# Kernel tuning notes

Measured on AMD Instinct MI355X. Metric: run time of the kernel, lower is better.

## Reference

```python
import jax, jax.numpy as jnp
import numpy as np

N_NODES = 100000
N_EDGES = 3200000
BATCH = 16
LAYER_NUMBER = 4


def setup_inputs() -> dict:
    key = jax.random.key(0)
    k1, k2, k3, k4 = jax.random.split(key, 4)
    x = jax.random.normal(k1, (N_NODES, BATCH), dtype=jnp.float32)
    # learnable per-edge weights (log1p(counts) at init in the original; the
    # parameter itself is what is learned, so a plain random init is faithful)
    weights = jax.random.normal(k2, (N_EDGES,), dtype=jnp.float32)
    row = jax.random.randint(k3, (N_EDGES,), 0, N_NODES, dtype=jnp.int64)
    col = jax.random.randint(k4, (N_EDGES,), 0, N_NODES, dtype=jnp.int64)
    return {"x": x, "weights": weights, "row": row, "col": col}


def reference(x, weights, row, col):
    # Repeated sparse COO SpMM: y <- A @ y, applied layer_number times,
    # where A[row[e], col[e]] = weights[e].
    def step(y, _):
        msg = weights[:, None] * y[col]                      # [E, B] gather + scale
        y_new = jax.ops.segment_sum(msg, row, num_segments=N_NODES)  # [N, B] scatter-add
        return y_new, None

    y, _ = jax.lax.scan(step, x, None, length=LAYER_NUMBER)
    return y
```

## Files before the change

kernel.cpp:

```cpp
#include <hip/hip_runtime.h>

#define N_NODES 100000
#define N_EDGES 3200000
#define BATCH 16
#define BKT_SHIFT 6
#define BKT_NODES 64
#define K_BUCKETS 1563
#define NB 512
#define SUB (N_EDGES / NB)
#define FT 512
#define SCAN_T 256
#define SCAN_C 7
#define CAP 4096

__global__ void hist_kernel(const int* __restrict__ row, int* __restrict__ blk_cnt) {
    __shared__ int lh[K_BUCKETS];
    int t = threadIdx.x, blk = blockIdx.x;
    for (int k = t; k < K_BUCKETS; k += 256) lh[k] = 0;
    __syncthreads();
    int base = blk * SUB;
    for (int e = base + t; e < base + SUB; e += 256)
        atomicAdd(&lh[row[e] >> BKT_SHIFT], 1);
    __syncthreads();
    for (int k = t; k < K_BUCKETS; k += 256)
        blk_cnt[k * NB + blk] = lh[k];
}

__global__ void colscan_kernel(int* __restrict__ blk_cnt, int* __restrict__ totals) {
    int wid = (blockIdx.x * blockDim.x + threadIdx.x) >> 6;
    int lane = threadIdx.x & 63;
    if (wid >= K_BUCKETS) return;
    int* p = &blk_cnt[wid * NB + lane * 8];
    int4 a = ((int4*)p)[0];
    int4 b = ((int4*)p)[1];
    int lt = a.x + a.y + a.z + a.w + b.x + b.y + b.z + b.w;
    int pref = lt;
    #pragma unroll
    for (int off = 1; off < 64; off <<= 1) {
        int v = __shfl_up(pref, off, 64);
        if (lane >= off) pref += v;
    }
    int run = pref - lt;
    int4 oa, ob;
    oa.x = run; run += a.x;
    oa.y = run; run += a.y;
    oa.z = run; run += a.z;
    oa.w = run; run += a.w;
    ob.x = run; run += b.x;
    ob.y = run; run += b.y;
    ob.z = run; run += b.z;
    ob.w = run; run += b.w;
    ((int4*)p)[0] = oa;
    ((int4*)p)[1] = ob;
    int tot = __shfl(pref, 63, 64);
    if (lane == 0) totals[wid] = tot;
}

__global__ void scan_kernel(const int* __restrict__ totals, int* __restrict__ bptr,
                            int* __restrict__ row_ptr) {
    __shared__ int s[SCAN_T];
    int t = threadIdx.x;
    int loc[SCAN_C];
    int sum = 0;
    for (int i = 0; i < SCAN_C; i++) {
        int idx = t * SCAN_C + i;
        int v = (idx < K_BUCKETS) ? totals[idx] : 0;
        loc[i] = v;
        sum += v;
    }
    s[t] = sum;
    __syncthreads();
    for (int off = 1; off < SCAN_T; off <<= 1) {
        int x = (t >= off) ? s[t - off] : 0;
        __syncthreads();
        s[t] += x;
        __syncthreads();
    }
    int excl = s[t] - sum;
    for (int i = 0; i < SCAN_C; i++) {
        int idx = t * SCAN_C + i;
        if (idx < K_BUCKETS) bptr[idx] = excl;
        excl += loc[i];
    }
    if (t == 0) { bptr[K_BUCKETS] = N_EDGES; row_ptr[N_NODES] = N_EDGES; }
}

__global__ void __launch_bounds__(FT) fill_kernel(
        const int* __restrict__ row, const int* __restrict__ col,
        const float* __restrict__ w,
        const int* __restrict__ bptr, const int* __restrict__ blk_cnt,
        uint2* __restrict__ entries) {
    __shared__ uint2 sbuf[SUB];
    __shared__ int lbeg[K_BUCKETS];
    __shared__ int lcur[K_BUCKETS];
    __shared__ int sscan[FT];
    int t = threadIdx.x, blk = blockIdx.x;
    for (int k = t; k < K_BUCKETS; k += FT) lcur[k] = 0;
    __syncthreads();
    int base = blk * SUB;
    for (int e = base + t; e < base + SUB; e += FT)
        atomicAdd(&lcur[row[e] >> BKT_SHIFT], 1);
    __syncthreads();
    int loc[4];
    int sum = 0;
    #pragma unroll
    for (int j = 0; j < 4; j++) {
        int k = t * 4 + j;
        int v = (k < K_BUCKETS) ? lcur[k] : 0;
        loc[j] = v;
        sum += v;
    }
    sscan[t] = sum;
    __syncthreads();
    for (int off = 1; off < FT; off <<= 1) {
        int x = (t >= off) ? sscan[t - off] : 0;
        __syncthreads();
        sscan[t] += x;
        __syncthreads();
    }
    int excl = sscan[t] - sum;
    #pragma unroll
    for (int j = 0; j < 4; j++) {
        int k = t * 4 + j;
        if (k < K_BUCKETS) { lbeg[k] = excl; lcur[k] = excl; }
        excl += loc[j];
    }
    __syncthreads();
    for (int e = base + t; e < base + SUB; e += FT) {
        int r = row[e];
        int bkt = r >> BKT_SHIFT;
        int pos = atomicAdd(&lcur[bkt], 1);
        sbuf[pos] = make_uint2(((unsigned)(r & (BKT_NODES - 1)) << 17) | (unsigned)col[e],
                               __float_as_uint(w[e]));
    }
    __syncthreads();
    int lane = t & 3;
    for (int k = (t >> 2); k < K_BUCKETS; k += FT / 4) {
        int lb = lbeg[k];
        int le = lcur[k];
        int dst = bptr[k] + blk_cnt[k * NB + blk];
        for (int i = lb + lane; i < le; i += 4)
            entries[dst + (i - lb)] = sbuf[i];
    }
}

__global__ void __launch_bounds__(256) nodesort_pull1_kernel(
        const int* __restrict__ bptr, uint2* __restrict__ entries,
        int* __restrict__ row_ptr,
        const float* __restrict__ x, float* __restrict__ out) {
    __shared__ uint2 ebuf[CAP];
    __shared__ int nh[BKT_NODES];
    __shared__ int nc[BKT_NODES];
    __shared__ int nstart[BKT_NODES + 1];
    int t = threadIdx.x, b = blockIdx.x;
    int beg = bptr[b], end = bptr[b + 1];
    int n = min(end - beg, CAP);
    if (t < BKT_NODES) nh[t] = 0;
    __syncthreads();
    uint2 rs[16];
    int cnt = 0;
    #pragma unroll
    for (int i = 0; i < 16; i++) {
        int k = t + i * 256;
        if (k < n) {
            uint2 r = entries[beg + k];
            rs[i] = r;
            atomicAdd(&nh[r.x >> 17], 1);
            cnt = i + 1;
        }
    }
    __syncthreads();
    if (t < BKT_NODES) {
        int v = nh[t];
        int pref = v;
        #pragma unroll
        for (int off = 1; off < BKT_NODES; off <<= 1) {
            int u = __shfl_up(pref, off, 64);
            if (t >= off) pref += u;
        }
        int excl = pref - v;
        nstart[t] = excl;
        nc[t] = excl;
        if (t == BKT_NODES - 1) nstart[BKT_NODES] = pref;
        int node = b * BKT_NODES + t;
        if (node < N_NODES) row_ptr[node] = beg + excl;
    }
    __syncthreads();
    #pragma unroll
    for (int i = 0; i < 16; i++) {
        if (i < cnt) {
            uint2 r = rs[i];
            int pos = atomicAdd(&nc[r.x >> 17], 1);
            ebuf[pos] = r;
            entries[beg + pos] = r;
        }
    }
    __syncthreads();
    int ln = t >> 2, q = t & 3;
    int node = b * BKT_NODES + ln;
    if (node >= N_NODES) return;
    int s = nstart[ln], e = nstart[ln + 1];
    float4 acc = make_float4(0.f, 0.f, 0.f, 0.f);
    int i = s;
    while (i + 8 <= e) {
        uint2 r0 = ebuf[i + 0], r1 = ebuf[i + 1], r2 = ebuf[i + 2], r3 = ebuf[i + 3];
        uint2 r4 = ebuf[i + 4], r5 = ebuf[i + 5], r6 = ebuf[i + 6], r7 = ebuf[i + 7];
        float4 y0 = *(const float4*)&x[(r0.x & 0x1FFFFu) * BATCH + q * 4];
        float4 y1 = *(const float4*)&x[(r1.x & 0x1FFFFu) * BATCH + q * 4];
        float4 y2 = *(const float4*)&x[(r2.x & 0x1FFFFu) * BATCH + q * 4];
        float4 y3 = *(const float4*)&x[(r3.x & 0x1FFFFu) * BATCH + q * 4];
        float4 y4 = *(const float4*)&x[(r4.x & 0x1FFFFu) * BATCH + q * 4];
        float4 y5 = *(const float4*)&x[(r5.x & 0x1FFFFu) * BATCH + q * 4];
        float4 y6 = *(const float4*)&x[(r6.x & 0x1FFFFu) * BATCH + q * 4];
        float4 y7 = *(const float4*)&x[(r7.x & 0x1FFFFu) * BATCH + q * 4];
        float w0 = __uint_as_float(r0.y), w1 = __uint_as_float(r1.y);
        float w2 = __uint_as_float(r2.y), w3 = __uint_as_float(r3.y);
        float w4 = __uint_as_float(r4.y), w5 = __uint_as_float(r5.y);
        float w6 = __uint_as_float(r6.y), w7 = __uint_as_float(r7.y);
        acc.x += w0 * y0.x; acc.y += w0 * y0.y; acc.z += w0 * y0.z; acc.w += w0 * y0.w;
        acc.x += w1 * y1.x; acc.y += w1 * y1.y; acc.z += w1 * y1.z; acc.w += w1 * y1.w;
        acc.x += w2 * y2.x; acc.y += w2 * y2.y; acc.z += w2 * y2.z; acc.w += w2 * y2.w;
        acc.x += w3 * y3.x; acc.y += w3 * y3.y; acc.z += w3 * y3.z; acc.w += w3 * y3.w;
        acc.x += w4 * y4.x; acc.y += w4 * y4.y; acc.z += w4 * y4.z; acc.w += w4 * y4.w;
        acc.x += w5 * y5.x; acc.y += w5 * y5.y; acc.z += w5 * y5.z; acc.w += w5 * y5.w;
        acc.x += w6 * y6.x; acc.y += w6 * y6.y; acc.z += w6 * y6.z; acc.w += w6 * y6.w;
        acc.x += w7 * y7.x; acc.y += w7 * y7.y; acc.z += w7 * y7.z; acc.w += w7 * y7.w;
        i += 8;
    }
    for (; i < e; i++) {
        uint2 r = ebuf[i];
        float4 yv = *(const float4*)&x[(r.x & 0x1FFFFu) * BATCH + q * 4];
        float wj = __uint_as_float(r.y);
        acc.x += wj * yv.x; acc.y += wj * yv.y;
        acc.z += wj * yv.z; acc.w += wj * yv.w;
    }
    *(float4*)&out[node * BATCH + q * 4] = acc;
}

__global__ void __launch_bounds__(256) pull_kernel(const float* __restrict__ y,
                            const uint2* __restrict__ entries,
                            const int* __restrict__ row_ptr,
                            float* __restrict__ out) {
    int tid = blockIdx.x * blockDim.x + threadIdx.x;
    int node = tid >> 2;
    int q = tid & 3;
    if (node >= N_NODES) return;
    int beg = row_ptr[node];
    int end = row_ptr[node + 1];
    float4 acc = make_float4(0.f, 0.f, 0.f, 0.f);
    if (beg < end) {
        int lim = end - 1;
        uint2 r[8];
        #pragma unroll
        for (int j = 0; j < 8; j++) r[j] = entries[min(beg + j, lim)];
        int i = beg;
        while (i + 8 <= end) {
            float4 yv[8];
            #pragma unroll
            for (int j = 0; j < 8; j++)
                yv[j] = *(const float4*)&y[(r[j].x & 0x1FFFFu) * BATCH + q * 4];
            uint2 nx[8];
            #pragma unroll
            for (int j = 0; j < 8; j++)
                nx[j] = entries[min(i + 8 + j, lim)];
            #pragma unroll
            for (int j = 0; j < 8; j++) {
                float wj = __uint_as_float(r[j].y);
                acc.x += wj * yv[j].x;
                acc.y += wj * yv[j].y;
                acc.z += wj * yv[j].z;
                acc.w += wj * yv[j].w;
            }
            #pragma unroll
            for (int j = 0; j < 8; j++) r[j] = nx[j];
            i += 8;
        }
        if (i < end) {
            float4 yv[8];
            #pragma unroll
            for (int j = 0; j < 8; j++)
                yv[j] = *(const float4*)&y[(r[j].x & 0x1FFFFu) * BATCH + q * 4];
            #pragma unroll
            for (int j = 0; j < 8; j++)
                if (i + j < end) {
                    float wj = __uint_as_float(r[j].y);
                    acc.x += wj * yv[j].x;
                    acc.y += wj * yv[j].y;
                    acc.z += wj * yv[j].z;
                    acc.w += wj * yv[j].w;
                }
        }
    }
    *(float4*)&out[node * BATCH + q * 4] = acc;
}

extern "C" void kernel_launch(void* const* d_in, const int* in_sizes, int n_in,
                              void* d_out, int out_size, void* d_ws, size_t ws_size,
                              hipStream_t stream) {
    const float* x   = (const float*)d_in[0];
    const float* w   = (const float*)d_in[1];
    const int*   row = (const int*)d_in[2];
    const int*   col = (const int*)d_in[3];
    float*       out = (float*)d_out;

    char* p = (char*)d_ws;
    uint2* entries = (uint2*)p;  p += (size_t)N_EDGES * sizeof(uint2);
    float* buf     = (float*)p;
    int*   blk_cnt = (int*)buf;
    p += (size_t)N_NODES * BATCH * sizeof(float);
    int* totals  = (int*)p;      p += 8192;
    int* bptr    = (int*)p;      p += 8192;
    int* row_ptr = (int*)p;

    hist_kernel<<<NB, 256, 0, stream>>>(row, blk_cnt);
    colscan_kernel<<<(K_BUCKETS * 64 + 255) / 256, 256, 0, stream>>>(blk_cnt, totals);
    scan_kernel<<<1, SCAN_T, 0, stream>>>(totals, bptr, row_ptr);
    fill_kernel<<<NB, FT, 0, stream>>>(row, col, w, bptr, blk_cnt, entries);

    nodesort_pull1_kernel<<<K_BUCKETS, 256, 0, stream>>>(bptr, entries, row_ptr, x, buf);
    const int pgrid = (N_NODES * 4 + 255) / 256;
    pull_kernel<<<pgrid, 256, 0, stream>>>(buf, entries, row_ptr, out);
    pull_kernel<<<pgrid, 256, 0, stream>>>(out, entries, row_ptr, buf);
    pull_kernel<<<pgrid, 256, 0, stream>>>(buf, entries, row_ptr, out);
}
```

Before: 316.2 us.

## Fuse CSR build phases into one cooperative kernel with grid syncs

Merges the histogram, column scan, bucket scan and fill kernels into a single cooperative kernel separated by grid-wide barriers. This removes three kernel launches and the duplicate histogram pass over row that the fill kernel used to recompute. The block-local shared-memory scans are replaced by wave shuffle scans. The cost is that all 512 blocks must be co-resident (launch bounds request 4 blocks per CU, with a large shared buffer), and each grid.sync plus threadfence adds a barrier.

Measured after the change: 750.9 us. +137.5%, slower.

```diff
diff --git a/kernel.cpp b/kernel.cpp
--- a/kernel.cpp
+++ b/kernel.cpp
@@ -1,4 +1,5 @@
 #include <hip/hip_runtime.h>
+#include <hip/hip_cooperative_groups.h>
 
 #define N_NODES 100000
 #define N_EDGES 3200000
@@ -9,98 +10,96 @@
 #define NB 512
 #define SUB (N_EDGES / NB)
 #define FT 512
-#define SCAN_T 256
-#define SCAN_C 7
 #define CAP 4096
 
-__global__ void hist_kernel(const int* __restrict__ row, int* __restrict__ blk_cnt) {
-    __shared__ int lh[K_BUCKETS];
-    int t = threadIdx.x, blk = blockIdx.x;
-    for (int k = t; k < K_BUCKETS; k += 256) lh[k] = 0;
-    __syncthreads();
-    int base = blk * SUB;
-    for (int e = base + t; e < base + SUB; e += 256)
-        atomicAdd(&lh[row[e] >> BKT_SHIFT], 1);
-    __syncthreads();
-    for (int k = t; k < K_BUCKETS; k += 256)
-        blk_cnt[k * NB + blk] = lh[k];
-}
-
-__global__ void colscan_kernel(int* __restrict__ blk_cnt, int* __restrict__ totals) {
-    int wid = (blockIdx.x * blockDim.x + threadIdx.x) >> 6;
-    int lane = threadIdx.x & 63;
-    if (wid >= K_BUCKETS) return;
-    int* p = &blk_cnt[wid * NB + lane * 8];
-    int4 a = ((int4*)p)[0];
-    int4 b = ((int4*)p)[1];
-    int lt = a.x + a.y + a.z + a.w + b.x + b.y + b.z + b.w;
-    int pref = lt;
-    #pragma unroll
-    for (int off = 1; off < 64; off <<= 1) {
-        int v = __shfl_up(pref, off, 64);
-        if (lane >= off) pref += v;
-    }
-    int run = pref - lt;
-    int4 oa, ob;
-    oa.x = run; run += a.x;
-    oa.y = run; run += a.y;
-    oa.z = run; run += a.z;
-    oa.w = run; run += a.w;
-    ob.x = run; run += b.x;
-    ob.y = run; run += b.y;
-    ob.z = run; run += b.z;
-    ob.w = run; run += b.w;
-    ((int4*)p)[0] = oa;
-    ((int4*)p)[1] = ob;
-    int tot = __shfl(pref, 63, 64);
-    if (lane == 0) totals[wid] = tot;
-}
-
-__global__ void scan_kernel(const int* __restrict__ totals, int* __restrict__ bptr,
-                            int* __restrict__ row_ptr) {
-    __shared__ int s[SCAN_T];
-    int t = threadIdx.x;
-    int loc[SCAN_C];
-    int sum = 0;
-    for (int i = 0; i < SCAN_C; i++) {
-        int idx = t * SCAN_C + i;
-        int v = (idx < K_BUCKETS) ? totals[idx] : 0;
-        loc[i] = v;
-        sum += v;
-    }
-    s[t] = sum;
-    __syncthreads();
-    for (int off = 1; off < SCAN_T; off <<= 1) {
-        int x = (t >= off) ? s[t - off] : 0;
-        __syncthreads();
-        s[t] += x;
-        __syncthreads();
-    }
-    int excl = s[t] - sum;
-    for (int i = 0; i < SCAN_C; i++) {
-        int idx = t * SCAN_C + i;
-        if (idx < K_BUCKETS) bptr[idx] = excl;
-        excl += loc[i];
-    }
-    if (t == 0) { bptr[K_BUCKETS] = N_EDGES; row_ptr[N_NODES] = N_EDGES; }
-}
-
-__global__ void __launch_bounds__(FT) fill_kernel(
+__global__ void __launch_bounds__(FT, 4) build_kernel(
         const int* __restrict__ row, const int* __restrict__ col,
         const float* __restrict__ w,
-        const int* __restrict__ bptr, const int* __restrict__ blk_cnt,
+        int* __restrict__ blk_cnt, int* __restrict__ totals,
+        int* __restrict__ bptr, int* __restrict__ row_ptr,
         uint2* __restrict__ entries) {
     __shared__ uint2 sbuf[SUB];
     __shared__ int lbeg[K_BUCKETS];
     __shared__ int lcur[K_BUCKETS];
-    __shared__ int sscan[FT];
+    __shared__ int cross[FT / 64];
+    cooperative_groups::grid_group grid = cooperative_groups::this_grid();
+
     int t = threadIdx.x, blk = blockIdx.x;
+    int lane = t & 63, wv = t >> 6;
+
     for (int k = t; k < K_BUCKETS; k += FT) lcur[k] = 0;
     __syncthreads();
     int base = blk * SUB;
     for (int e = base + t; e < base + SUB; e += FT)
         atomicAdd(&lcur[row[e] >> BKT_SHIFT], 1);
     __syncthreads();
+    for (int k = t; k < K_BUCKETS; k += FT)
+        blk_cnt[k * NB + blk] = lcur[k];
+    __threadfence();
+    grid.sync();
+
+    int wave = blk * (FT / 64) + wv;
+    if (wave < K_BUCKETS) {
+        int* p = &blk_cnt[wave * NB + lane * 8];
+        int4 a = ((int4*)p)[0];
+        int4 b = ((int4*)p)[1];
+        int lt = a.x + a.y + a.z + a.w + b.x + b.y + b.z + b.w;
+        int pref = lt;
+        #pragma unroll
+        for (int off = 1; off < 64; off <<= 1) {
+            int v = __shfl_up(pref, off, 64);
+            if (lane >= off) pref += v;
+        }
+        int run = pref - lt;
+        int4 oa, ob;
+        oa.x = run; run += a.x;
+        oa.y = run; run += a.y;
+        oa.z = run; run += a.z;
+        oa.w = run; run += a.w;
+        ob.x = run; run += b.x;
+        ob.y = run; run += b.y;
+        ob.z = run; run += b.z;
+        ob.w = run; run += b.w;
+        ((int4*)p)[0] = oa;
+        ((int4*)p)[1] = ob;
+        int tot = __shfl(pref, 63, 64);
+        if (lane == 0) totals[wave] = tot;
+    }
+    __threadfence();
+    grid.sync();
+
+    if (blk == 0) {
+        int loc[4];
+        int sum = 0;
+        #pragma unroll
+        for (int i = 0; i < 4; i++) {
+            int idx = t * 4 + i;
+            int v = (idx < K_BUCKETS) ? totals[idx] : 0;
+            loc[i] = v;
+            sum += v;
+        }
+        int pref = sum;
+        #pragma unroll
+        for (int off = 1; off < 64; off <<= 1) {
+            int u = __shfl_up(pref, off, 64);
+            if (lane >= off) pref += u;
+        }
+        if (lane == 63) cross[wv] = pref;
+        __syncthreads();
+        int wbase = 0;
+        for (int i = 0; i < wv; i++) wbase += cross[i];
+        int excl = wbase + pref - sum;
+        #pragma unroll
+        for (int i = 0; i < 4; i++) {
+            int idx = t * 4 + i;
+            if (idx < K_BUCKETS) bptr[idx] = excl;
+            excl += loc[i];
+        }
+        if (t == 0) { bptr[K_BUCKETS] = N_EDGES; row_ptr[N_NODES] = N_EDGES; }
+    }
+    __threadfence();
+    grid.sync();
+
     int loc[4];
     int sum = 0;
     #pragma unroll
@@ -110,15 +109,17 @@
         loc[j] = v;
         sum += v;
     }
-    sscan[t] = sum;
-    __syncthreads();
-    for (int off = 1; off < FT; off <<= 1) {
-        int x = (t >= off) ? sscan[t - off] : 0;
-        __syncthreads();
-        sscan[t] += x;
-        __syncthreads();
-    }
-    int excl = sscan[t] - sum;
+    int pref = sum;
+    #pragma unroll
+    for (int off = 1; off < 64; off <<= 1) {
+        int u = __shfl_up(pref, off, 64);
+        if (lane >= off) pref += u;
+    }
+    if (lane == 63) cross[wv] = pref;
+    __syncthreads();
+    int wbase = 0;
+    for (int i = 0; i < wv; i++) wbase += cross[i];
+    int excl = wbase + pref - sum;
     #pragma unroll
     for (int j = 0; j < 4; j++) {
         int k = t * 4 + j;
@@ -134,12 +135,12 @@
                                __float_as_uint(w[e]));
     }
     __syncthreads();
-    int lane = t & 3;
+    int cl = t & 3;
     for (int k = (t >> 2); k < K_BUCKETS; k += FT / 4) {
         int lb = lbeg[k];
         int le = lcur[k];
         int dst = bptr[k] + blk_cnt[k * NB + blk];
-        for (int i = lb + lane; i < le; i += 4)
+        for (int i = lb + cl; i < le; i += 4)
             entries[dst + (i - lb)] = sbuf[i];
     }
 }
@@ -312,10 +313,11 @@
     int* bptr    = (int*)p;      p += 8192;
     int* row_ptr = (int*)p;
 
-    hist_kernel<<<NB, 256, 0, stream>>>(row, blk_cnt);
-    colscan_kernel<<<(K_BUCKETS * 64 + 255) / 256, 256, 0, stream>>>(blk_cnt, totals);
-    scan_kernel<<<1, SCAN_T, 0, stream>>>(totals, bptr, row_ptr);
-    fill_kernel<<<NB, FT, 0, stream>>>(row, col, w, bptr, blk_cnt, entries);
+    void* args[] = { (void*)&row, (void*)&col, (void*)&w,
+                     (void*)&blk_cnt, (void*)&totals,
+                     (void*)&bptr, (void*)&row_ptr, (void*)&entries };
+    hipLaunchCooperativeKernel((void*)build_kernel, dim3(NB), dim3(FT),
+                               args, 0, stream);
 
     nodesort_pull1_kernel<<<K_BUCKETS, 256, 0, stream>>>(bptr, entries, row_ptr, x, buf);
     const int pgrid = (N_NODES * 4 + 255) / 256;
```
